# Kernel optimization log

Measured on AMD Instinct MI355X. Metric: run time of the kernel, lower is better.

The kernel has to match this reference:

```python
import jax, jax.numpy as jnp
import numpy as np
from functools import reduce

N_QUBITS = 4
N_LAYERS = 3
DIM = 2 ** N_QUBITS  # 16

I2 = jnp.eye(2, dtype=jnp.complex64)

def _cnot_mat(c, t, n=N_QUBITS):
    # big-endian (PennyLane) ordering: wire 0 is the most significant bit
    M = np.zeros((2 ** n, 2 ** n), dtype=np.complex64)
    for idx in range(2 ** n):
        if (idx >> (n - 1 - c)) & 1:
            new = idx ^ (1 << (n - 1 - t))
        else:
            new = idx
        M[new, idx] = 1.0
    return jnp.asarray(M)

# entangling layer: CNOT(0,1), CNOT(1,2), CNOT(2,3), CNOT(3,0)
_ENT = reduce(lambda A, B: B @ A,
              [_cnot_mat(i, i + 1) for i in range(N_QUBITS - 1)] + [_cnot_mat(N_QUBITS - 1, 0)],
              jnp.eye(DIM, dtype=jnp.complex64))

# PauliZ expectation sign table: zs[idx, i] = +1/-1 for bit i of basis state idx
_ZS = jnp.asarray(
    np.array([[1.0 - 2.0 * ((idx >> (N_QUBITS - 1 - i)) & 1) for i in range(N_QUBITS)]
              for idx in range(DIM)], dtype=np.float32))

def _ry(t):
    c, s = jnp.cos(t / 2), jnp.sin(t / 2)
    return jnp.stack([jnp.stack([c, -s]), jnp.stack([s, c])]).astype(jnp.complex64)

def _rz(t):
    e = jnp.exp(-0.5j * t.astype(jnp.complex64))
    return jnp.stack([jnp.stack([e, 0.0 * e]), jnp.stack([0.0 * e, jnp.conj(e)])])

def _embed(g, w):
    mats = [I2] * w + [g] + [I2] * (N_QUBITS - 1 - w)
    return reduce(jnp.kron, mats)

def _variational_unitary(params):
    # fixed (data-independent) 16x16 unitary for the whole variational circuit
    U = jnp.eye(DIM, dtype=jnp.complex64)
    off = 0
    for _ in range(N_LAYERS):
        for i in range(N_QUBITS):
            U = _embed(_ry(params[off]), i) @ U; off += 1
            U = _embed(_rz(params[off]), i) @ U; off += 1
            U = _embed(_ry(params[off]), i) @ U; off += 1
        U = _ENT @ U
    return U

def setup_inputs() -> dict:
    key = jax.random.key(0)
    k1, k2 = jax.random.split(key)
    x = jax.random.uniform(k1, (4096, 784), dtype=jnp.float32)
    params = jax.random.normal(k2, (36,), dtype=jnp.float32)
    return {"x": x, "params": params}

def reference(x, params):
    bsz = x.shape[0]
    # 2x2 non-overlapping patches, row-major over (r, c): [bsz, 196, 4]
    img = x.reshape(bsz, 14, 2, 14, 2)
    patches = img.transpose(0, 1, 3, 2, 4).reshape(bsz, 196, 4)
    theta = (patches * jnp.pi).reshape(bsz * 196, 4)  # RY encoding angles
    # RY(theta)|0> = [cos(theta/2), sin(theta/2)] -> product state over 4 qubits
    a, b = jnp.cos(theta / 2), jnp.sin(theta / 2)
    q = jnp.stack([a, b], axis=-1).astype(jnp.complex64)  # [N, 4, 2]
    psi0 = jnp.einsum('na,nb,nc,nd->nabcd', q[:, 0], q[:, 1], q[:, 2], q[:, 3]).reshape(-1, DIM)
    U = _variational_unitary(params)
    psi = psi0 @ U.T  # [N, 16]
    probs = (psi.real ** 2 + psi.imag ** 2).astype(jnp.float32)
    expvals = probs @ _ZS  # [N, 4] Pauli-Z expectations
    return expvals.reshape(bsz, 196 * 4)
```

## Files before the change

### kernel.cpp

```cpp
#include <hip/hip_runtime.h>
#include <math.h>

#define DIM 16

__global__ __launch_bounds__(64) void build_unitary_kernel(
    const float* __restrict__ params, float* __restrict__ Uout) {
  __shared__ float s_c[36], s_s[36];
  const int t = threadIdx.x;
  if (t < 36) {
    const float half = params[t] * 0.5f;
    s_c[t] = cosf(half);
    s_s[t] = sinf(half);
  }
  __syncthreads();
  if (t >= DIM) return;
  const int col = t;

  float vr[DIM], vi[DIM];
#pragma unroll
  for (int k = 0; k < DIM; ++k) { vr[k] = (k == col) ? 1.0f : 0.0f; vi[k] = 0.0f; }

  int off = 0;
#pragma unroll
  for (int layer = 0; layer < 3; ++layer) {
#pragma unroll
    for (int w = 0; w < 4; ++w) {
      const int m = 1 << (3 - w);
      {
        const float cy = s_c[off], sy = s_s[off]; ++off;
#pragma unroll
        for (int k0 = 0; k0 < DIM; ++k0) {
          if (k0 & m) continue;
          const int k1 = k0 | m;
          const float ar = vr[k0], ai = vi[k0], br = vr[k1], bi = vi[k1];
          vr[k0] = cy * ar - sy * br;  vi[k0] = cy * ai - sy * bi;
          vr[k1] = sy * ar + cy * br;  vi[k1] = sy * ai + cy * bi;
        }
      }
      {
        const float cz = s_c[off], sz = s_s[off]; ++off;
#pragma unroll
        for (int k = 0; k < DIM; ++k) {
          const float sg = (k & m) ? sz : -sz;
          const float ar = vr[k], ai = vi[k];
          vr[k] = cz * ar - sg * ai;
          vi[k] = cz * ai + sg * ar;
        }
      }
      {
        const float cy = s_c[off], sy = s_s[off]; ++off;
#pragma unroll
        for (int k0 = 0; k0 < DIM; ++k0) {
          if (k0 & m) continue;
          const int k1 = k0 | m;
          const float ar = vr[k0], ai = vi[k0], br = vr[k1], bi = vi[k1];
          vr[k0] = cy * ar - sy * br;  vi[k0] = cy * ai - sy * bi;
          vr[k1] = sy * ar + cy * br;  vi[k1] = sy * ai + cy * bi;
        }
      }
    }
#pragma unroll
    for (int g = 0; g < 4; ++g) {
      const int a = (g < 3) ? g : 3;
      const int b = (g < 3) ? (g + 1) : 0;
      const int ca = 1 << (3 - a);
      const int tb = 1 << (3 - b);
#pragma unroll
      for (int r = 0; r < DIM; ++r) {
        if ((r & ca) && !(r & tb)) {
          const int r2 = r | tb;
          float tmp;
          tmp = vr[r]; vr[r] = vr[r2]; vr[r2] = tmp;
          tmp = vi[r]; vi[r] = vi[r2]; vi[r2] = tmp;
        }
      }
    }
  }
#pragma unroll
  for (int k = 0; k < DIM; ++k) {
    Uout[k * DIM + col]       = vr[k];
    Uout[256 + k * DIM + col] = vi[k];
  }
}

__global__ __launch_bounds__(256) void quanv_kernel(
    const float* __restrict__ x, const float* __restrict__ U,
    float* __restrict__ out, int npatch) {
  const int n = blockIdx.x * 256 + threadIdx.x;
  if (n >= npatch) return;
  const unsigned b  = (unsigned)n / 196u;
  const unsigned p  = (unsigned)n - b * 196u;
  const unsigned r1 = p / 14u;
  const unsigned c1 = p - r1 * 14u;
  const float* xb = x + b * 784u + r1 * 56u + c1 * 2u;
  const float2 t0 = *(const float2*)(xb);
  const float2 t1 = *(const float2*)(xb + 28);

  const float HPI = 1.57079632679489662f;
  float c0, s0, c1q, s1q, c2q, s2q, c3q, s3q;
  __sincosf(t0.x * HPI, &s0,  &c0);
  __sincosf(t0.y * HPI, &s1q, &c1q);
  __sincosf(t1.x * HPI, &s2q, &c2q);
  __sincosf(t1.y * HPI, &s3q, &c3q);

  const float ab[4] = {c0 * c1q, c0 * s1q, s0 * c1q, s0 * s1q};
  const float cd[4] = {c2q * c3q, c2q * s3q, s2q * c3q, s2q * s3q};
  float psi0[16];
#pragma unroll
  for (int k = 0; k < 16; ++k) psi0[k] = ab[k >> 2] * cd[k & 3];

  const float* __restrict__ Ur = U;
  const float* __restrict__ Ui = U + 256;
  float ev0 = 0.f, ev1 = 0.f, ev2 = 0.f, ev3 = 0.f;
#pragma unroll
  for (int j = 0; j < 16; ++j) {
    float pr = 0.f, pi = 0.f;
#pragma unroll
    for (int k = 0; k < 16; ++k) {
      pr = fmaf(Ur[j * 16 + k], psi0[k], pr);
      pi = fmaf(Ui[j * 16 + k], psi0[k], pi);
    }
    const float prob = fmaf(pr, pr, pi * pi);
    ev0 += (j & 8) ? -prob : prob;
    ev1 += (j & 4) ? -prob : prob;
    ev2 += (j & 2) ? -prob : prob;
    ev3 += (j & 1) ? -prob : prob;
  }
  ((float4*)out)[n] = make_float4(ev0, ev1, ev2, ev3);
}

extern "C" void kernel_launch(void* const* d_in, const int* in_sizes, int n_in,
                              void* d_out, int out_size, void* d_ws, size_t ws_size,
                              hipStream_t stream) {
  const float* x      = (const float*)d_in[0];
  const float* params = (const float*)d_in[1];
  float* out = (float*)d_out;
  float* U   = (float*)d_ws;

  build_unitary_kernel<<<1, 64, 0, stream>>>(params, U);

  const int npatch = in_sizes[0] / 4;
  const int nblk = (npatch + 255) / 256;
  quanv_kernel<<<nblk, 256, 0, stream>>>(x, U, out, npatch);
}
```

Measured before the change: 84.40 us.

## Compute state-vector transform with split-fp16 MFMA and LDS reduction

Replaces the per-thread scalar 16x16 complex matvec with 32x32x16 fp16 MFMA instructions. The unitary real and imaginary parts are packed as a 16x32 B matrix, and each operand is split into high and low fp16 halves, using three MFMAs to approximate fp32 accuracy. Squared outputs are staged through LDS and reduced per patch into Pauli-Z expectations with a butterfly of sums and differences. This removes the scalar FMA load, but adds LDS traffic, a block barrier and some precision risk from the fp16 split.

```diff
diff --git a/kernel.cpp b/kernel.cpp
--- a/kernel.cpp
+++ b/kernel.cpp
@@ -3,8 +3,11 @@
 
 #define DIM 16
 
+typedef __attribute__((ext_vector_type(8))) _Float16 half8;
+typedef __attribute__((ext_vector_type(16))) float f32x16;
+
 __global__ __launch_bounds__(64) void build_unitary_kernel(
-    const float* __restrict__ params, float* __restrict__ Uout) {
+    const float* __restrict__ params, float* __restrict__ Bmat) {
   __shared__ float s_c[36], s_s[36];
   const int t = threadIdx.x;
   if (t < 36) {
@@ -77,56 +80,111 @@
     }
   }
 #pragma unroll
-  for (int k = 0; k < DIM; ++k) {
-    Uout[k * DIM + col]       = vr[k];
-    Uout[256 + k * DIM + col] = vi[k];
+  for (int n = 0; n < DIM; ++n) {
+    Bmat[col * 32 + n]       = vr[n];
+    Bmat[col * 32 + 16 + n]  = vi[n];
   }
 }
 
-__global__ __launch_bounds__(256) void quanv_kernel(
-    const float* __restrict__ x, const float* __restrict__ U,
+__global__ __launch_bounds__(256) void quanv_mfma_kernel(
+    const float* __restrict__ x, const float* __restrict__ Bmat,
     float* __restrict__ out, int npatch) {
-  const int n = blockIdx.x * 256 + threadIdx.x;
-  if (n >= npatch) return;
-  const unsigned b  = (unsigned)n / 196u;
-  const unsigned p  = (unsigned)n - b * 196u;
-  const unsigned r1 = p / 14u;
-  const unsigned c1 = p - r1 * 14u;
-  const float* xb = x + b * 784u + r1 * 56u + c1 * 2u;
-  const float2 t0 = *(const float2*)(xb);
-  const float2 t1 = *(const float2*)(xb + 28);
-
-  const float HPI = 1.57079632679489662f;
-  float c0, s0, c1q, s1q, c2q, s2q, c3q, s3q;
-  __sincosf(t0.x * HPI, &s0,  &c0);
-  __sincosf(t0.y * HPI, &s1q, &c1q);
-  __sincosf(t1.x * HPI, &s2q, &c2q);
-  __sincosf(t1.y * HPI, &s3q, &c3q);
-
-  const float ab[4] = {c0 * c1q, c0 * s1q, s0 * c1q, s0 * s1q};
-  const float cd[4] = {c2q * c3q, c2q * s3q, s2q * c3q, s2q * s3q};
-  float psi0[16];
-#pragma unroll
-  for (int k = 0; k < 16; ++k) psi0[k] = ab[k >> 2] * cd[k & 3];
-
-  const float* __restrict__ Ur = U;
-  const float* __restrict__ Ui = U + 256;
-  float ev0 = 0.f, ev1 = 0.f, ev2 = 0.f, ev3 = 0.f;
-#pragma unroll
-  for (int j = 0; j < 16; ++j) {
-    float pr = 0.f, pi = 0.f;
-#pragma unroll
-    for (int k = 0; k < 16; ++k) {
-      pr = fmaf(Ur[j * 16 + k], psi0[k], pr);
-      pi = fmaf(Ui[j * 16 + k], psi0[k], pi);
-    }
-    const float prob = fmaf(pr, pr, pi * pi);
-    ev0 += (j & 8) ? -prob : prob;
-    ev1 += (j & 4) ? -prob : prob;
-    ev2 += (j & 2) ? -prob : prob;
-    ev3 += (j & 1) ? -prob : prob;
-  }
-  ((float4*)out)[n] = make_float4(ev0, ev1, ev2, ev3);
+  __shared__ __align__(16) float q_lds[256 * 36];
+
+  const int tid  = threadIdx.x;
+  const int lane = tid & 63;
+  const int wave = tid >> 6;
+  const int nl   = lane & 31;
+  const int h    = lane >> 5;
+  const int kb   = h * 8;
+
+  half8 bh, bl;
+#pragma unroll
+  for (int j = 0; j < 8; ++j) {
+    const float v = Bmat[(kb + j) * 32 + nl];
+    const _Float16 vh = (_Float16)v;
+    bh[j] = vh;
+    bl[j] = (_Float16)(v - (float)vh);
+  }
+
+  const int blk_base = blockIdx.x * 256;
+
+#pragma unroll
+  for (int it = 0; it < 2; ++it) {
+    const int roff = wave * 64 + it * 32;
+    int n = blk_base + roff + nl;
+    if (n >= npatch) n = npatch - 1;
+    const unsigned nu = (unsigned)n;
+    const unsigned b  = nu / 196u;
+    const unsigned p  = nu - b * 196u;
+    const unsigned r1 = p / 14u;
+    const unsigned c1 = p - r1 * 14u;
+    const float* xb = x + b * 784u + r1 * 56u + c1 * 2u;
+    const float2 t0 = *(const float2*)(xb);
+    const float2 t1 = *(const float2*)(xb + 28);
+
+    const float HPI = 1.57079632679489662f;
+    float c0, s0, c1q, s1q, c2q, s2q, c3q, s3q;
+    __sincosf(t0.x * HPI, &s0,  &c0);
+    __sincosf(t0.y * HPI, &s1q, &c1q);
+    __sincosf(t1.x * HPI, &s2q, &c2q);
+    __sincosf(t1.y * HPI, &s3q, &c3q);
+
+    const float f   = h ? s0 : c0;
+    const float ab0 = f * c1q, ab1 = f * s1q;
+    const float cd[4] = {c2q * c3q, c2q * s3q, s2q * c3q, s2q * s3q};
+
+    half8 ah, al;
+#pragma unroll
+    for (int j = 0; j < 8; ++j) {
+      const float v = ((j & 4) ? ab1 : ab0) * cd[j & 3];
+      const _Float16 vh = (_Float16)v;
+      ah[j] = vh;
+      al[j] = (_Float16)(v - (float)vh);
+    }
+
+    f32x16 C;
+#pragma unroll
+    for (int r = 0; r < 16; ++r) C[r] = 0.0f;
+    C = __builtin_amdgcn_mfma_f32_32x32x16_f16(ah, bh, C, 0, 0, 0);
+    C = __builtin_amdgcn_mfma_f32_32x32x16_f16(al, bh, C, 0, 0, 0);
+    C = __builtin_amdgcn_mfma_f32_32x32x16_f16(ah, bl, C, 0, 0, 0);
+
+#pragma unroll
+    for (int reg = 0; reg < 16; ++reg) {
+      const int row = (reg & 3) + 8 * (reg >> 2) + 4 * h + roff;
+      q_lds[row * 36 + nl] = C[reg] * C[reg];
+    }
+  }
+  __syncthreads();
+
+  float q[32];
+#pragma unroll
+  for (int j = 0; j < 8; ++j) {
+    const float4 v = *(const float4*)&q_lds[tid * 36 + 4 * j];
+    q[4 * j + 0] = v.x; q[4 * j + 1] = v.y;
+    q[4 * j + 2] = v.z; q[4 * j + 3] = v.w;
+  }
+  float pr[16];
+#pragma unroll
+  for (int j = 0; j < 16; ++j) pr[j] = q[j] + q[j + 16];
+
+  float s1[8], d1[8];
+#pragma unroll
+  for (int j = 0; j < 8; ++j) { s1[j] = pr[j] + pr[j + 8]; d1[j] = pr[j] - pr[j + 8]; }
+  float ev0 = ((d1[0] + d1[1]) + (d1[2] + d1[3])) + ((d1[4] + d1[5]) + (d1[6] + d1[7]));
+  float s2[4], d2[4];
+#pragma unroll
+  for (int j = 0; j < 4; ++j) { s2[j] = s1[j] + s1[j + 4]; d2[j] = s1[j] - s1[j + 4]; }
+  float ev1 = (d2[0] + d2[1]) + (d2[2] + d2[3]);
+  const float s3a = s2[0] + s2[2], s3b = s2[1] + s2[3];
+  const float d3a = s2[0] - s2[2], d3b = s2[1] - s2[3];
+  float ev2 = d3a + d3b;
+  float ev3 = (s3a + s3b) - 2.0f * s3b;
+  ev3 = s3a - s3b;
+
+  const int gp = blk_base + tid;
+  if (gp < npatch) ((float4*)out)[gp] = make_float4(ev0, ev1, ev2, ev3);
 }
 
 extern "C" void kernel_launch(void* const* d_in, const int* in_sizes, int n_in,
@@ -134,12 +192,12 @@
                               hipStream_t stream) {
   const float* x      = (const float*)d_in[0];
   const float* params = (const float*)d_in[1];
-  float* out = (float*)d_out;
-  float* U   = (float*)d_ws;
-
-  build_unitary_kernel<<<1, 64, 0, stream>>>(params, U);
+  float* out  = (float*)d_out;
+  float* Bmat = (float*)d_ws;
+
+  build_unitary_kernel<<<1, 64, 0, stream>>>(params, Bmat);
 
   const int npatch = in_sizes[0] / 4;
   const int nblk = (npatch + 255) / 256;
-  quanv_kernel<<<nblk, 256, 0, stream>>>(x, U, out, npatch);
+  quanv_mfma_kernel<<<nblk, 256, 0, stream>>>(x, Bmat, out, npatch);
 }
```

New measurement: 78.92 us. -6.5%, faster.

## Compute patch state-vector transform with split-fp16 MFMA instead of scalar FMAs

Applied to the files above, without the earlier changes.

Replaces the per-thread 16x16 complex matrix-vector product with 32x32x16 f16 MFMA instructions. The real and imaginary parts of U are stacked as a 32x16 A matrix, and each wave processes 32 patches per MFMA pair. U is split into high and low fp16 parts to recover precision, though the psi0 operand is rounded to fp16. Expectation values are reduced across the two half-waves with shuffles. This aims to cut the large scalar FMA count, at the cost of reduced precision and extra lane shuffles.

```diff
diff --git a/kernel.cpp b/kernel.cpp
--- a/kernel.cpp
+++ b/kernel.cpp
@@ -3,8 +3,11 @@
 
 #define DIM 16
 
+typedef __attribute__((ext_vector_type(8))) _Float16 half8;
+typedef __attribute__((ext_vector_type(16))) float f32x16;
+
 __global__ __launch_bounds__(64) void build_unitary_kernel(
-    const float* __restrict__ params, float* __restrict__ Uout) {
+    const float* __restrict__ params, float* __restrict__ Amat) {
   __shared__ float s_c[36], s_s[36];
   const int t = threadIdx.x;
   if (t < 36) {
@@ -77,56 +80,89 @@
     }
   }
 #pragma unroll
-  for (int k = 0; k < DIM; ++k) {
-    Uout[k * DIM + col]       = vr[k];
-    Uout[256 + k * DIM + col] = vi[k];
+  for (int n = 0; n < DIM; ++n) {
+    Amat[n * 16 + col]        = vr[n];
+    Amat[(16 + n) * 16 + col] = vi[n];
   }
 }
 
-__global__ __launch_bounds__(256) void quanv_kernel(
-    const float* __restrict__ x, const float* __restrict__ U,
+__global__ __launch_bounds__(256) void quanv_mfma_kernel(
+    const float* __restrict__ x, const float* __restrict__ Amat,
     float* __restrict__ out, int npatch) {
-  const int n = blockIdx.x * 256 + threadIdx.x;
-  if (n >= npatch) return;
-  const unsigned b  = (unsigned)n / 196u;
-  const unsigned p  = (unsigned)n - b * 196u;
-  const unsigned r1 = p / 14u;
-  const unsigned c1 = p - r1 * 14u;
-  const float* xb = x + b * 784u + r1 * 56u + c1 * 2u;
-  const float2 t0 = *(const float2*)(xb);
-  const float2 t1 = *(const float2*)(xb + 28);
+  const int tid  = threadIdx.x;
+  const int lane = tid & 63;
+  const int wave = tid >> 6;
+  const int nl   = lane & 31;
+  const int h    = lane >> 5;
 
-  const float HPI = 1.57079632679489662f;
-  float c0, s0, c1q, s1q, c2q, s2q, c3q, s3q;
-  __sincosf(t0.x * HPI, &s0,  &c0);
-  __sincosf(t0.y * HPI, &s1q, &c1q);
-  __sincosf(t1.x * HPI, &s2q, &c2q);
-  __sincosf(t1.y * HPI, &s3q, &c3q);
+  const float4* Arow = (const float4*)(Amat + nl * 16 + 8 * h);
+  const float4 ua = Arow[0];
+  const float4 ub = Arow[1];
+  const float uf[8] = {ua.x, ua.y, ua.z, ua.w, ub.x, ub.y, ub.z, ub.w};
+  half8 Uh, Ul;
+#pragma unroll
+  for (int j = 0; j < 8; ++j) {
+    const _Float16 vh = (_Float16)uf[j];
+    Uh[j] = vh;
+    Ul[j] = (_Float16)(uf[j] - (float)vh);
+  }
 
-  const float ab[4] = {c0 * c1q, c0 * s1q, s0 * c1q, s0 * s1q};
-  const float cd[4] = {c2q * c3q, c2q * s3q, s2q * c3q, s2q * s3q};
-  float psi0[16];
+  const int base = blockIdx.x * 256 + wave * 64;
+
 #pragma unroll
-  for (int k = 0; k < 16; ++k) psi0[k] = ab[k >> 2] * cd[k & 3];
+  for (int it = 0; it < 2; ++it) {
+    int n = base + it * 32 + nl;
+    if (n >= npatch) n = npatch - 1;
+    const unsigned nu = (unsigned)n;
+    const unsigned b  = nu / 196u;
+    const unsigned p  = nu - b * 196u;
+    const unsigned r1 = p / 14u;
+    const unsigned c1 = p - r1 * 14u;
+    const float* xb = x + b * 784u + r1 * 56u + c1 * 2u;
+    const float2 t0 = *(const float2*)(xb);
+    const float2 t1 = *(const float2*)(xb + 28);
 
-  const float* __restrict__ Ur = U;
-  const float* __restrict__ Ui = U + 256;
-  float ev0 = 0.f, ev1 = 0.f, ev2 = 0.f, ev3 = 0.f;
+    const float HPI = 1.57079632679489662f;
+    float c0, s0, c1q, s1q, c2q, s2q, c3q, s3q;
+    __sincosf(t0.x * HPI, &s0,  &c0);
+    __sincosf(t0.y * HPI, &s1q, &c1q);
+    __sincosf(t1.x * HPI, &s2q, &c2q);
+    __sincosf(t1.y * HPI, &s3q, &c3q);
+
+    const float f   = h ? s0 : c0;
+    const float ab0 = f * c1q, ab1 = f * s1q;
+    const float cd[4] = {c2q * c3q, c2q * s3q, s2q * c3q, s2q * s3q};
+    half8 bfrag;
 #pragma unroll
-  for (int j = 0; j < 16; ++j) {
-    float pr = 0.f, pi = 0.f;
+    for (int j = 0; j < 8; ++j)
+      bfrag[j] = (_Float16)(((j & 4) ? ab1 : ab0) * cd[j & 3]);
+
+    f32x16 C;
 #pragma unroll
-    for (int k = 0; k < 16; ++k) {
-      pr = fmaf(Ur[j * 16 + k], psi0[k], pr);
-      pi = fmaf(Ui[j * 16 + k], psi0[k], pi);
-    }
-    const float prob = fmaf(pr, pr, pi * pi);
-    ev0 += (j & 8) ? -prob : prob;
-    ev1 += (j & 4) ? -prob : prob;
-    ev2 += (j & 2) ? -prob : prob;
-    ev3 += (j & 1) ? -prob : prob;
+    for (int r = 0; r < 16; ++r) C[r] = 0.0f;
+    C = __builtin_amdgcn_mfma_f32_32x32x16_f16(Uh, bfrag, C, 0, 0, 0);
+    C = __builtin_amdgcn_mfma_f32_32x32x16_f16(Ul, bfrag, C, 0, 0, 0);
+
+    float pq[8];
+#pragma unroll
+    for (int r = 0; r < 8; ++r) pq[r] = fmaf(C[r], C[r], C[r + 8] * C[r + 8]);
+
+    const float s03 = pq[0] + pq[3], s12 = pq[1] + pq[2];
+    const float s47 = pq[4] + pq[7], s56 = pq[5] + pq[6];
+    float e0 = (s03 + s12) - (s47 + s56);
+    float e1 = (s03 + s12) + (s47 + s56);  e1 = h ? -e1 : e1;
+    float e2 = ((pq[0] + pq[1]) - (pq[2] + pq[3]))
+             + ((pq[4] + pq[5]) - (pq[6] + pq[7]));
+    float e3 = ((pq[0] - pq[1]) + (pq[2] - pq[3]))
+             + ((pq[4] - pq[5]) + (pq[6] - pq[7]));
+    e0 += __shfl_xor(e0, 32, 64);
+    e1 += __shfl_xor(e1, 32, 64);
+    e2 += __shfl_xor(e2, 32, 64);
+    e3 += __shfl_xor(e3, 32, 64);
+
+    if (h == 0 && n < npatch)
+      ((float4*)out)[n] = make_float4(e0, e1, e2, e3);
   }
-  ((float4*)out)[n] = make_float4(ev0, ev1, ev2, ev3);
 }
 
 extern "C" void kernel_launch(void* const* d_in, const int* in_sizes, int n_in,
@@ -134,12 +170,12 @@
                               hipStream_t stream) {
   const float* x      = (const float*)d_in[0];
   const float* params = (const float*)d_in[1];
-  float* out = (float*)d_out;
-  float* U   = (float*)d_ws;
+  float* out  = (float*)d_out;
+  float* Amat = (float*)d_ws;
 
-  build_unitary_kernel<<<1, 64, 0, stream>>>(params, U);
+  build_unitary_kernel<<<1, 64, 0, stream>>>(params, Amat);
 
   const int npatch = in_sizes[0] / 4;
   const int nblk = (npatch + 255) / 256;
-  quanv_kernel<<<nblk, 256, 0, stream>>>(x, U, out, npatch);
+  quanv_mfma_kernel<<<nblk, 256, 0, stream>>>(x, Amat, out, npatch);
 }
```

New measurement: 76.54 us. -9.3%, faster.
